# Kernel optimization log

Hardware: AMD Instinct MI355X
Metric: run time of the kernel (lower is better)

## Reference

```python
import jax, jax.numpy as jnp
import numpy as np

B, L, D = 16, 1024, 768

def setup_inputs() -> dict:
    key = jax.random.key(0)
    k1, k2, k3, k4 = jax.random.split(key, 4)
    d_embedding = jax.random.normal(k1, (B, L, D), dtype=jnp.float32)
    d_mask = jax.random.randint(k2, (B, L), 0, 2) == 1
    W = jax.random.normal(k3, (D, D), dtype=jnp.float32) / np.sqrt(D)
    b = jax.random.normal(k4, (D,), dtype=jnp.float32) * 0.01
    return {"d_embedding": d_embedding, "d_mask": d_mask, "W": W, "b": b}

def reference(d_embedding, d_mask, W, b):
    # linear + relu projection: [B, L, D]
    p = jax.nn.relu(jnp.einsum('bld,de->ble', d_embedding, W.T) + b)
    # self-attention scores: [B, L, L]
    scores = jnp.einsum('bld,bmd->blm', p, p)
    # zero out the diagonal (multiply by (1 - eye))
    diag_off = 1.0 - jnp.eye(L, dtype=scores.dtype)
    scores = scores * diag_off[None, :, :]
    # mask padded key positions with -inf (columns)
    scores = jnp.where(d_mask[:, None, :], -jnp.inf, scores)
    # softmax over keys
    alpha = jax.nn.softmax(scores, axis=-1)  # [B, L, L]
    align_feature = jnp.einsum('blm,bmd->bld', alpha, d_embedding)
    return align_feature, alpha
```

## Files before the change

### kernel.cpp

```cpp
#include <hip/hip_runtime.h>
#include <math.h>

#define B_ 16
#define L_ 1024
#define D_ 768

typedef short bf16x8 __attribute__((ext_vector_type(8)));
typedef _Float16 half8 __attribute__((ext_vector_type(8)));
typedef float f32x4 __attribute__((ext_vector_type(4)));

__device__ __forceinline__ unsigned short f2bf(float x) {
  unsigned u = __float_as_uint(x);
  u = (u + 0x7FFFu + ((u >> 16) & 1u)) >> 16;
  return (unsigned short)u;
}
__device__ __forceinline__ float bf2f(unsigned short h) {
  return __uint_as_float(((unsigned)h) << 16);
}
__device__ __forceinline__ unsigned short f2h(float x) {
  union { _Float16 h; unsigned short u; } v;
  v.h = (_Float16)x;
  return v.u;
}

__global__ __launch_bounds__(256) void k_mask2(const void* __restrict__ mraw,
                                               int* __restrict__ canon,
                                               int* __restrict__ psum,
                                               int* __restrict__ kinfo) {
  __shared__ int flags[2];
  __shared__ int tsum[256];
  const int b = blockIdx.x;
  const int tid = threadIdx.x;
  if (tid < 2) flags[tid] = 0;
  __syncthreads();
  const unsigned* m32 = (const unsigned*)mraw;
  int gt = 0, oddnz = 0;
  for (int i = tid; i < 4096; i += 256) {
    unsigned v = m32[i];
    if (v > 1u) gt = 1;
    if ((i & 1) && v != 0u) oddnz = 1;
  }
  if (gt) atomicOr(&flags[0], 1);
  if (oddnz) atomicOr(&flags[1], 1);
  __syncthreads();
  const int mode = flags[0] ? 0 : (flags[1] ? 1 : 2);
  int v[4];
#pragma unroll
  for (int e = 0; e < 4; ++e) {
    const int i = b * L_ + tid * 4 + e;
    int mv;
    if (mode == 0)      mv = ((const unsigned char*)mraw)[i];
    else if (mode == 1) mv = ((const int*)mraw)[i];
    else                mv = (int)(((const long long*)mraw)[i] != 0);
    v[e] = (mv != 0);
    canon[i] = v[e];
  }
  const int vc = (1 - v[0]) + (1 - v[1]) + (1 - v[2]) + (1 - v[3]);
  tsum[tid] = vc;
  __syncthreads();
  for (int off = 1; off < 256; off <<= 1) {
    const int t = (tid >= off) ? tsum[tid - off] : 0;
    __syncthreads();
    tsum[tid] += t;
    __syncthreads();
  }
  int run = tsum[tid] - vc;
#pragma unroll
  for (int e = 0; e < 4; ++e) {
    psum[b * L_ + tid * 4 + e] = run;
    run += 1 - v[e];
  }
  if (tid == 255) {
    const int tot = tsum[255];
    kinfo[b] = (tot + 63) >> 6;
    kinfo[16 + b] = tot;
  }
}

__global__ __launch_bounds__(256) void k_prep16(const float* __restrict__ X,
                                                unsigned short* __restrict__ Xf,
                                                unsigned short* __restrict__ Xt,
                                                const int* __restrict__ psum,
                                                const int* __restrict__ canon) {
  __shared__ unsigned short t16[64][66];
  const int b = blockIdx.z;
  const int d0 = blockIdx.x * 64, m0 = blockIdx.y * 64;
  const int dd = threadIdx.x & 63, mq = threadIdx.x >> 6;
#pragma unroll
  for (int i = 0; i < 16; ++i) {
    const int m = mq * 16 + i;
    const size_t gidx = ((size_t)b * L_ + m0 + m) * D_ + d0 + dd;
    const unsigned short h = f2h(X[gidx]);
    Xf[gidx] = h;
    t16[dd][m] = h;
  }
  __syncthreads();
  const int mm = threadIdx.x & 63, dq = threadIdx.x >> 6;
  const int gm = m0 + mm;
  if (!canon[b * L_ + gm]) {
    const int j = psum[b * L_ + gm];
#pragma unroll
    for (int i = 0; i < 16; ++i) {
      const int d = dq * 16 + i;
      Xt[((size_t)b * D_ + d0 + d) * L_ + j] = t16[d][mm];
    }
  }
}

__global__ __launch_bounds__(256) void k_prep(const float* __restrict__ X,
                                              unsigned short* __restrict__ Xh,
                                              unsigned short* __restrict__ Xl,
                                              unsigned short* __restrict__ Xt) {
  __shared__ unsigned short t16[64][66];
  const int b = blockIdx.z;
  const int d0 = blockIdx.x * 64, m0 = blockIdx.y * 64;
  const int dd = threadIdx.x & 63, mq = threadIdx.x >> 6;
#pragma unroll
  for (int i = 0; i < 16; ++i) {
    const int m = mq * 16 + i;
    const size_t gidx = ((size_t)b * L_ + m0 + m) * D_ + d0 + dd;
    const float x = X[gidx];
    const unsigned short h = f2bf(x);
    Xh[gidx] = h;
    Xl[gidx] = f2bf(x - bf2f(h));
    t16[dd][m] = h;
  }
  __syncthreads();
  const int mm = threadIdx.x & 63, dq = threadIdx.x >> 6;
#pragma unroll
  for (int i = 0; i < 16; ++i) {
    const int d = dq * 16 + i;
    Xt[((size_t)b * D_ + d0 + d) * L_ + m0 + mm] = t16[d][mm];
  }
}

__global__ __launch_bounds__(256) void k_pad(unsigned short* __restrict__ Xtc,
                                             unsigned short* __restrict__ a16c,
                                             const int* __restrict__ kinfo) {
  const int b = blockIdx.x;
  const int nt64 = kinfo[b] * 64;
  const int kv = kinfo[16 + b];
  if (kv >= nt64) return;
  const int r = blockIdx.y * 64 + (threadIdx.x >> 2);
  const int cg = threadIdx.x & 3;
  unsigned short* base = (r < 768)
      ? Xtc + ((size_t)b * D_ + r) * L_
      : a16c + ((size_t)b * L_ + (r - 768)) * L_;
#pragma unroll
  for (int q = 0; q < 16; ++q) {
    const int c = kv + cg * 16 + q;
    if (c < nt64) base[c] = 0;
  }
}

__global__ __launch_bounds__(256) void k_castW(const float* __restrict__ W,
                                               unsigned short* __restrict__ Wf,
                                               int n8) {
  const int i = blockIdx.x * 256 + threadIdx.x;
  if (i >= n8) return;
  const float4 a = *(const float4*)(W + (size_t)i * 8);
  const float4 b = *(const float4*)(W + (size_t)i * 8 + 4);
  *(ushort4*)(Wf + (size_t)i * 8)     = make_ushort4(f2h(a.x), f2h(a.y), f2h(a.z), f2h(a.w));
  *(ushort4*)(Wf + (size_t)i * 8 + 4) = make_ushort4(f2h(b.x), f2h(b.y), f2h(b.z), f2h(b.w));
}

__device__ __forceinline__ void stage_panel(const unsigned short* __restrict__ ph,
                                            const unsigned short* __restrict__ pl,
                                            size_t grow0, int kk,
                                            char* ldsbase, int wave, int lane) {
#pragma unroll
  for (int q = 0; q < 4; ++q) {
    const int s = wave * 4 + q;
    const int row = s * 8 + (lane >> 3);
    const int xs = (lane & 7) ^ (row & 7);
    const unsigned short* src = (xs & 4) ? pl : ph;
    const unsigned short* g = src + (grow0 + row) * D_ + kk + (xs & 3) * 8;
    __builtin_amdgcn_global_load_lds(
        (const __attribute__((address_space(1))) void*)g,
        (__attribute__((address_space(3))) void*)(ldsbase + s * 1024),
        16, 0, 0);
  }
}

__device__ __forceinline__ void stage_panel1(const unsigned short* __restrict__ g0,
                                             size_t rstride,
                                             char* ldsbase, int wave, int lane) {
#pragma unroll
  for (int q = 0; q < 4; ++q) {
    const int s = wave * 4 + q;
    const int row = s * 8 + (lane >> 3);
    const int xs = (lane & 7) ^ (row & 7);
    const unsigned short* g = g0 + (size_t)row * rstride + xs * 8;
    __builtin_amdgcn_global_load_lds(
        (const __attribute__((address_space(1))) void*)g,
        (__attribute__((address_space(3))) void*)(ldsbase + s * 1024),
        16, 0, 0);
  }
}

__device__ __forceinline__ bf16x8 ldsfrag(const char* base, int row, int g) {
  return *(const bf16x8*)(base + row * 128 + ((g ^ (row & 7)) * 16));
}
__device__ __forceinline__ half8 ldsfrag_h(const char* base, int row, int g) {
  return *(const half8*)(base + row * 128 + ((g ^ (row & 7)) * 16));
}

__global__ __launch_bounds__(256) void k_proj3(const unsigned short* __restrict__ Xf,
                                               const unsigned short* __restrict__ Wf,
                                               const float* __restrict__ bias,
                                               unsigned short* __restrict__ Pf) {
  __shared__ __align__(16) char smem[49152];
  const int tid = threadIdx.x;
  const int xcd = (int)blockIdx.x & 7;
  const int li  = (int)blockIdx.x >> 3;
  const int m0 = (xcd * 16 + li / 6) * 128;
  const int n0 = (li % 6) * 128;
  const int lane = tid & 63, wave = tid >> 6;
  const int wr = wave >> 1, wc = wave & 1;
  const int fr = lane & 15, kg = lane >> 4;
  f32x4 acc[4][4];
#pragma unroll
  for (int i = 0; i < 4; ++i)
#pragma unroll
    for (int j = 0; j < 4; ++j) acc[i][j] = 0;

  const unsigned short* a0 = Xf + (size_t)m0 * D_;
  const unsigned short* b0 = Wf + (size_t)n0 * D_;

  stage_panel1(a0, D_, smem, wave, lane);
  stage_panel1(b0, D_, smem + 32768, wave, lane);
  __syncthreads();

  int cur = 0;
  for (int it = 0; it < D_ / 64; ++it) {
    const char* ab = smem + cur * 16384;
    const char* bb = smem + 32768;
    half8 fa[2][4], fb[2][4];
#pragma unroll
    for (int i = 0; i < 4; ++i) {
      const int ra = wr * 64 + i * 16 + fr;
      const int rb = wc * 64 + i * 16 + fr;
#pragma unroll
      for (int ks = 0; ks < 2; ++ks) {
        fa[ks][i] = ldsfrag_h(ab, ra, ks * 4 + kg);
        fb[ks][i] = ldsfrag_h(bb, rb, ks * 4 + kg);
      }
    }
    __syncthreads();
    if (it + 1 < D_ / 64) {
      stage_panel1(a0 + (it + 1) * 64, D_, smem + (cur ^ 1) * 16384, wave, lane);
      stage_panel1(b0 + (it + 1) * 64, D_, smem + 32768, wave, lane);
    }
#pragma unroll
    for (int ks = 0; ks < 2; ++ks)
#pragma unroll
      for (int i = 0; i < 4; ++i)
#pragma unroll
        for (int j = 0; j < 4; ++j)
          acc[i][j] = __builtin_amdgcn_mfma_f32_16x16x32_f16(fa[ks][i], fb[ks][j],
                                                             acc[i][j], 0, 0, 0);
    __syncthreads();
    cur ^= 1;
  }

  unsigned short* scr = (unsigned short*)smem + wave * 1152;
  const int row = lane >> 2, seg = lane & 3;
  float bj[4];
#pragma unroll
  for (int j = 0; j < 4; ++j) bj[j] = bias[n0 + wc * 64 + j * 16 + fr];
  for (int i = 0; i < 4; ++i) {
    __syncthreads();
#pragma unroll
    for (int j = 0; j < 4; ++j)
#pragma unroll
      for (int r = 0; r < 4; ++r)
        scr[(kg * 4 + r) * 72 + j * 16 + fr] = f2h(fmaxf(acc[i][j][r] + bj[j], 0.f));
    __syncthreads();
    const size_t gr = (size_t)(m0 + wr * 64 + i * 16 + row);
    const int gc0 = n0 + wc * 64 + seg * 16;
    const uint4 h0 = *(const uint4*)&scr[row * 72 + seg * 16];
    const uint4 h1 = *(const uint4*)&scr[row * 72 + seg * 16 + 8];
    *(uint4*)(Pf + gr * D_ + gc0)     = h0;
    *(uint4*)(Pf + gr * D_ + gc0 + 8) = h1;
  }
}

__global__ __launch_bounds__(256) void k_proj(const float* __restrict__ X,
                                              const float* __restrict__ W,
                                              const float* __restrict__ bias,
                                              unsigned short* __restrict__ Ph,
                                              unsigned short* __restrict__ Pl) {
  __shared__ __align__(16) unsigned short smem[4 * 128 * 32];
  unsigned short (*Ah)[32] = (unsigned short(*)[32])smem;
  unsigned short (*Al)[32] = (unsigned short(*)[32])(smem + 1 * 128 * 32);
  unsigned short (*Bh)[32] = (unsigned short(*)[32])(smem + 2 * 128 * 32);
  unsigned short (*Bl)[32] = (unsigned short(*)[32])(smem + 3 * 128 * 32);

  const int tid = threadIdx.x;
  const int swz = ((int)blockIdx.x % 8) * 96 + (int)blockIdx.x / 8;
  const int m0 = (swz / 6) * 128, n0 = (swz % 6) * 128;
  const int lane = tid & 63, wave = tid >> 6;
  const int wr = wave >> 1, wc = wave & 1;
  const int fr = lane & 15, kg = lane >> 4;
  f32x4 acc[4][4];
#pragma unroll
  for (int i = 0; i < 4; ++i)
#pragma unroll
    for (int j = 0; j < 4; ++j) acc[i][j] = 0;

  float4 av[4], bv[4];
#pragma unroll
  for (int p = 0; p < 4; ++p) {
    const int f = tid + p * 256, r = f >> 3, c = f & 7;
    av[p] = *(const float4*)(X + (size_t)(m0 + r) * D_ + c * 4);
    bv[p] = *(const float4*)(W + (size_t)(n0 + r) * D_ + c * 4);
  }

  for (int it = 0; it < D_ / 32; ++it) {
    __syncthreads();
#pragma unroll
    for (int p = 0; p < 4; ++p) {
      const int f = tid + p * 256, r = f >> 3, c = f & 7;
      {
        const float x0 = av[p].x, x1 = av[p].y, x2 = av[p].z, x3 = av[p].w;
        const unsigned short h0 = f2bf(x0), h1 = f2bf(x1), h2 = f2bf(x2), h3 = f2bf(x3);
        *(ushort4*)&Ah[r][c * 4] = make_ushort4(h0, h1, h2, h3);
        *(ushort4*)&Al[r][c * 4] = make_ushort4(f2bf(x0 - bf2f(h0)), f2bf(x1 - bf2f(h1)),
                                                f2bf(x2 - bf2f(h2)), f2bf(x3 - bf2f(h3)));
      }
      {
        const float x0 = bv[p].x, x1 = bv[p].y, x2 = bv[p].z, x3 = bv[p].w;
        const unsigned short h0 = f2bf(x0), h1 = f2bf(x1), h2 = f2bf(x2), h3 = f2bf(x3);
        *(ushort4*)&Bh[r][c * 4] = make_ushort4(h0, h1, h2, h3);
        *(ushort4*)&Bl[r][c * 4] = make_ushort4(f2bf(x0 - bf2f(h0)), f2bf(x1 - bf2f(h1)),
                                                f2bf(x2 - bf2f(h2)), f2bf(x3 - bf2f(h3)));
      }
    }
    __syncthreads();
    if (it + 1 < D_ / 32) {
      const int kk = (it + 1) * 32;
#pragma unroll
      for (int p = 0; p < 4; ++p) {
        const int f = tid + p * 256, r = f >> 3, c = f & 7;
        av[p] = *(const float4*)(X + (size_t)(m0 + r) * D_ + kk + c * 4);
        bv[p] = *(const float4*)(W + (size_t)(n0 + r) * D_ + kk + c * 4);
      }
    }
    bf16x8 fah[4], fal[4], fbh[4], fbl[4];
#pragma unroll
    for (int i = 0; i < 4; ++i) {
      fah[i] = *(const bf16x8*)&Ah[wr * 64 + i * 16 + fr][kg * 8];
      fal[i] = *(const bf16x8*)&Al[wr * 64 + i * 16 + fr][kg * 8];
      fbh[i] = *(const bf16x8*)&Bh[wc * 64 + i * 16 + fr][kg * 8];
      fbl[i] = *(const bf16x8*)&Bl[wc * 64 + i * 16 + fr][kg * 8];
    }
#pragma unroll
    for (int i = 0; i < 4; ++i)
#pragma unroll
      for (int j = 0; j < 4; ++j) {
        acc[i][j] = __builtin_amdgcn_mfma_f32_16x16x32_bf16(fah[i], fbh[j], acc[i][j], 0, 0, 0);
        acc[i][j] = __builtin_amdgcn_mfma_f32_16x16x32_bf16(fah[i], fbl[j], acc[i][j], 0, 0, 0);
        acc[i][j] = __builtin_amdgcn_mfma_f32_16x16x32_bf16(fal[i], fbh[j], acc[i][j], 0, 0, 0);
      }
  }

  unsigned short* scr = smem + wave * 2304;
  const int row = lane >> 2, seg = lane & 3;
  float bj[4];
#pragma unroll
  for (int j = 0; j < 4; ++j) bj[j] = bias[n0 + wc * 64 + j * 16 + fr];
  for (int i = 0; i < 4; ++i) {
    __syncthreads();
#pragma unroll
    for (int j = 0; j < 4; ++j)
#pragma unroll
      for (int r = 0; r < 4; ++r) {
        float v = fmaxf(acc[i][j][r] + bj[j], 0.f);
        const unsigned short h = f2bf(v);
        scr[(kg * 4 + r) * 72 + j * 16 + fr] = h;
        scr[1152 + (kg * 4 + r) * 72 + j * 16 + fr] = f2bf(v - bf2f(h));
      }
    __syncthreads();
    const size_t gr = (size_t)(m0 + wr * 64 + i * 16 + row);
    const int gc0 = n0 + wc * 64 + seg * 16;
    const uint4 h0 = *(const uint4*)&scr[row * 72 + seg * 16];
    const uint4 h1 = *(const uint4*)&scr[row * 72 + seg * 16 + 8];
    const uint4 q0 = *(const uint4*)&scr[1152 + row * 72 + seg * 16];
    const uint4 q1 = *(const uint4*)&scr[1152 + row * 72 + seg * 16 + 8];
    *(uint4*)(Ph + gr * D_ + gc0)     = h0;
    *(uint4*)(Ph + gr * D_ + gc0 + 8) = h1;
    *(uint4*)(Pl + gr * D_ + gc0)     = q0;
    *(uint4*)(Pl + gr * D_ + gc0 + 8) = q1;
  }
}

__global__ __launch_bounds__(256) void k_scores(const unsigned short* __restrict__ Pf,
                                                const int* __restrict__ mask,
                                                float* __restrict__ S) {
  __shared__ __align__(16) char smem[65536];

  const int tid = threadIdx.x;
  const int swz = ((int)blockIdx.x % 8) * 72 + (int)blockIdx.x / 8;
  const int bb = swz / 36;
  const int pr = swz % 36;
  int ti = 0;
  while ((ti + 1) * (ti + 2) / 2 <= pr) ++ti;
  const int tj = pr - ti * (ti + 1) / 2;
  const int l0 = ti * 128, m0 = tj * 128;
  const int lane = tid & 63, wave = tid >> 6;
  const int wr = wave >> 1, wc = wave & 1;
  const int fr = lane & 15, kg = lane >> 4;
  f32x4 acc[4][4];
#pragma unroll
  for (int i = 0; i < 4; ++i)
#pragma unroll
    for (int j = 0; j < 4; ++j) acc[i][j] = 0;

  const unsigned short* a0 = Pf + ((size_t)bb * L_ + l0) * D_;
  const unsigned short* b0 = Pf + ((size_t)bb * L_ + m0) * D_;

  stage_panel1(a0, D_, smem, wave, lane);
  stage_panel1(b0, D_, smem + 16384, wave, lane);
  __syncthreads();

  int cur = 0;
  for (int it = 0; it < D_ / 64; ++it) {
    char* cb = smem + cur * 32768;
    if (it + 1 < D_ / 64) {
      char* nb = smem + (cur ^ 1) * 32768;
      stage_panel1(a0 + (it + 1) * 64, D_, nb, wave, lane);
      stage_panel1(b0 + (it + 1) * 64, D_, nb + 16384, wave, lane);
    }
    half8 fa[2][4], fb[2][4];
#pragma unroll
    for (int i = 0; i < 4; ++i) {
      const int ra = wr * 64 + i * 16 + fr;
      const int rb = wc * 64 + i * 16 + fr;
#pragma unroll
      for (int ks = 0; ks < 2; ++ks) {
        fa[ks][i] = ldsfrag_h(cb, ra, ks * 4 + kg);
        fb[ks][i] = ldsfrag_h(cb + 16384, rb, ks * 4 + kg);
      }
    }
#pragma unroll
    for (int ks = 0; ks < 2; ++ks)
#pragma unroll
      for (int i = 0; i < 4; ++i)
#pragma unroll
        for (int j = 0; j < 4; ++j)
          acc[i][j] = __builtin_amdgcn_mfma_f32_16x16x32_f16(fa[ks][i], fb[ks][j],
                                                             acc[i][j], 0, 0, 0);
    __syncthreads();
    cur ^= 1;
  }

  float* scr = (float*)smem + wave * 1280;
  const int row = lane >> 2, seg = lane & 3;
  for (int i = 0; i < 4; ++i) {
    __syncthreads();
#pragma unroll
    for (int j = 0; j < 4; ++j)
#pragma unroll
      for (int r = 0; r < 4; ++r)
        scr[(kg * 4 + r) * 68 + j * 16 + fr] = acc[i][j][r];
    __syncthreads();
    const int gl = l0 + wr * 64 + i * 16 + row;
    const int gm0 = m0 + wc * 64 + seg * 16;
    const size_t sbase = ((size_t)bb * L_ + gl) * L_ + gm0;
#pragma unroll
    for (int t = 0; t < 4; ++t) {
      float4 o = *(const float4*)&scr[row * 68 + seg * 16 + t * 4];
      const int4 mk = *(const int4*)(mask + bb * L_ + gm0 + t * 4);
      float* op = (float*)&o;
      const int* mp = (const int*)&mk;
#pragma unroll
      for (int e = 0; e < 4; ++e) {
        const int gm = gm0 + t * 4 + e;
        if (gm == gl) op[e] = 0.f;
        if (mp[e]) op[e] = -INFINITY;
      }
      *(float4*)(S + sbase + t * 4) = o;
    }
  }

  if (ti != tj) {
    __syncthreads();
#pragma unroll
    for (int j = 0; j < 4; ++j) {
      const int mloc = wc * 64 + j * 16 + fr;
#pragma unroll
      for (int i = 0; i < 4; ++i) {
        const int slot = wr * 16 + i * 4 + kg;
        const int xs = slot ^ (mloc & 7);
        *(f32x4*)(smem + mloc * 512 + xs * 16) = acc[i][j];
      }
    }
    __syncthreads();
    const int mrow = tid >> 1, half = tid & 1;
    const size_t sbase = ((size_t)bb * L_ + m0 + mrow) * L_ + l0;
#pragma unroll
    for (int q = 0; q < 16; ++q) {
      const int slot = half * 16 + q;
      const int xs = slot ^ (mrow & 7);
      float4 o = *(const float4*)(smem + mrow * 512 + xs * 16);
      const int4 mk = *(const int4*)(mask + bb * L_ + l0 + slot * 4);
      if (mk.x) o.x = -INFINITY;
      if (mk.y) o.y = -INFINITY;
      if (mk.z) o.z = -INFINITY;
      if (mk.w) o.w = -INFINITY;
      *(float4*)(S + sbase + slot * 4) = o;
    }
  }
}

__global__ __launch_bounds__(256) void k_scores_bf(const unsigned short* __restrict__ Ph,
                                                   const unsigned short* __restrict__ Pl,
                                                   const int* __restrict__ mask,
                                                   float* __restrict__ S) {
  __shared__ __align__(16) char smem[65536];

  const int tid = threadIdx.x;
  const int swz = ((int)blockIdx.x % 8) * 72 + (int)blockIdx.x / 8;
  const int bb = swz / 36;
  const int pr = swz % 36;
  int ti = 0;
  while ((ti + 1) * (ti + 2) / 2 <= pr) ++ti;
  const int tj = pr - ti * (ti + 1) / 2;
  const int l0 = ti * 128, m0 = tj * 128;
  const int lane = tid & 63, wave = tid >> 6;
  const int wr = wave >> 1, wc = wave & 1;
  const int fr = lane & 15, kg = lane >> 4;
  f32x4 acc[4][4];
#pragma unroll
  for (int i = 0; i < 4; ++i)
#pragma unroll
    for (int j = 0; j < 4; ++j) acc[i][j] = 0;

  const size_t arow0 = (size_t)bb * L_ + l0;
  const size_t brow0 = (size_t)bb * L_ + m0;

  stage_panel(Ph, Pl, arow0, 0, smem, wave, lane);
  stage_panel(Ph, Pl, brow0, 0, smem + 16384, wave, lane);
  __syncthreads();

  int cur = 0;
  for (int it = 0; it < D_ / 32; ++it) {
    char* cb = smem + cur * 32768;
    if (it + 1 < D_ / 32) {
      char* nb = smem + (cur ^ 1) * 32768;
      stage_panel(Ph, Pl, arow0, (it + 1) * 32, nb, wave, lane);
      stage_panel(Ph, Pl, brow0, (it + 1) * 32, nb + 16384, wave, lane);
    }
    bf16x8 fah[4], fal[4], fbh[4], fbl[4];
#pragma unroll
    for (int i = 0; i < 4; ++i) {
      const int ra = wr * 64 + i * 16 + fr;
      const int rb = wc * 64 + i * 16 + fr;
      fah[i] = ldsfrag(cb, ra, kg);
      fal[i] = ldsfrag(cb, ra, kg + 4);
      fbh[i] = ldsfrag(cb + 16384, rb, kg);
      fbl[i] = ldsfrag(cb + 16384, rb, kg + 4);
    }
#pragma unroll
    for (int i = 0; i < 4; ++i)
#pragma unroll
      for (int j = 0; j < 4; ++j) {
        acc[i][j] = __builtin_amdgcn_mfma_f32_16x16x32_bf16(fah[i], fbh[j], acc[i][j], 0, 0, 0);
        acc[i][j] = __builtin_amdgcn_mfma_f32_16x16x32_bf16(fah[i], fbl[j], acc[i][j], 0, 0, 0);
        acc[i][j] = __builtin_amdgcn_mfma_f32_16x16x32_bf16(fal[i], fbh[j], acc[i][j], 0, 0, 0);
      }
    __syncthreads();
    cur ^= 1;
  }

  float* scr = (float*)smem + wave * 1280;
  const int row = lane >> 2, seg = lane & 3;
  for (int i = 0; i < 4; ++i) {
    __syncthreads();
#pragma unroll
    for (int j = 0; j < 4; ++j)
#pragma unroll
      for (int r = 0; r < 4; ++r)
        scr[(kg * 4 + r) * 68 + j * 16 + fr] = acc[i][j][r];
    __syncthreads();
    const int gl = l0 + wr * 64 + i * 16 + row;
    const int gm0 = m0 + wc * 64 + seg * 16;
    const size_t sbase = ((size_t)bb * L_ + gl) * L_ + gm0;
#pragma unroll
    for (int t = 0; t < 4; ++t) {
      float4 o = *(const float4*)&scr[row * 68 + seg * 16 + t * 4];
      const int4 mk = *(const int4*)(mask + bb * L_ + gm0 + t * 4);
      float* op = (float*)&o;
      const int* mp = (const int*)&mk;
#pragma unroll
      for (int e = 0; e < 4; ++e) {
        const int gm = gm0 + t * 4 + e;
        if (gm == gl) op[e] = 0.f;
        if (mp[e]) op[e] = -INFINITY;
      }
      *(float4*)(S + sbase + t * 4) = o;
    }
  }

  if (ti != tj) {
    __syncthreads();
#pragma unroll
    for (int j = 0; j < 4; ++j) {
      const int mloc = wc * 64 + j * 16 + fr;
#pragma unroll
      for (int i = 0; i < 4; ++i) {
        const int slot = wr * 16 + i * 4 + kg;
        const int xs = slot ^ (mloc & 7);
        *(f32x4*)(smem + mloc * 512 + xs * 16) = acc[i][j];
      }
    }
    __syncthreads();
    const int mrow = tid >> 1, half = tid & 1;
    const size_t sbase = ((size_t)bb * L_ + m0 + mrow) * L_ + l0;
#pragma unroll
    for (int q = 0; q < 16; ++q) {
      const int slot = half * 16 + q;
      const int xs = slot ^ (mrow & 7);
      float4 o = *(const float4*)(smem + mrow * 512 + xs * 16);
      const int4 mk = *(const int4*)(mask + bb * L_ + l0 + slot * 4);
      if (mk.x) o.x = -INFINITY;
      if (mk.y) o.y = -INFINITY;
      if (mk.z) o.z = -INFINITY;
      if (mk.w) o.w = -INFINITY;
      *(float4*)(S + sbase + slot * 4) = o;
    }
  }
}

__global__ __launch_bounds__(256) void k_softmax(float* __restrict__ S,
                                                 unsigned short* __restrict__ a16,
                                                 const int* __restrict__ psum,
                                                 const int* __restrict__ canon) {
  const size_t row = blockIdx.x;
  float4* rp = (float4*)(S + row * L_);
  float4 v = rp[threadIdx.x];
  float mx = fmaxf(fmaxf(v.x, v.y), fmaxf(v.z, v.w));
#pragma unroll
  for (int o = 32; o > 0; o >>= 1) mx = fmaxf(mx, __shfl_xor(mx, o));
  __shared__ float rmax[4], rsum[4];
  const int wv = threadIdx.x >> 6, ln = threadIdx.x & 63;
  if (ln == 0) rmax[wv] = mx;
  __syncthreads();
  mx = fmaxf(fmaxf(rmax[0], rmax[1]), fmaxf(rmax[2], rmax[3]));
  float4 e;
  e.x = __expf(v.x - mx); e.y = __expf(v.y - mx);
  e.z = __expf(v.z - mx); e.w = __expf(v.w - mx);
  float s = (e.x + e.y) + (e.z + e.w);
#pragma unroll
  for (int o = 32; o > 0; o >>= 1) s += __shfl_xor(s, o);
  if (ln == 0) rsum[wv] = s;
  __syncthreads();
  s = (rsum[0] + rsum[1]) + (rsum[2] + rsum[3]);
  const float inv = 1.0f / s;
  e.x *= inv; e.y *= inv; e.z *= inv; e.w *= inv;
  rp[threadIdx.x] = e;
  if (a16) {
    const int bbat = (int)(row >> 10);
    const int m0 = threadIdx.x * 4;
    const int4 mk = *(const int4*)(canon + bbat * L_ + m0);
    const int4 ps = *(const int4*)(psum + bbat * L_ + m0);
    unsigned short* arow = a16 + row * L_;
    if (!mk.x) arow[ps.x] = f2h(e.x);
    if (!mk.y) arow[ps.y] = f2h(e.y);
    if (!mk.z) arow[ps.z] = f2h(e.z);
    if (!mk.w) arow[ps.w] = f2h(e.w);
  }
}

__global__ __launch_bounds__(256) void k_align2(const unsigned short* __restrict__ A16,
                                                const unsigned short* __restrict__ Xt,
                                                const int* __restrict__ kinfo,
                                                float* __restrict__ O) {
  __shared__ __align__(16) char smem[65536];
  const int tid = threadIdx.x;
  const int swz = ((int)blockIdx.x % 8) * 96 + (int)blockIdx.x / 8;
  const int bb = swz / 48;
  const int l0 = ((swz / 6) % 8) * 128;
  const int n0 = (swz % 6) * 128;
  const int nt = kinfo[bb];
  const int lane = tid & 63, wave = tid >> 6;
  const int wr = wave >> 1, wc = wave & 1;
  const int fr = lane & 15, kg = lane >> 4;
  f32x4 acc[4][4];
#pragma unroll
  for (int i = 0; i < 4; ++i)
#pragma unroll
    for (int j = 0; j < 4; ++j) acc[i][j] = 0;

  const unsigned short* a0 = A16 + ((size_t)bb * L_ + l0) * L_;
  const unsigned short* b0 = Xt + ((size_t)bb * D_ + n0) * L_;

  if (nt > 0) {
    stage_panel1(a0, L_, smem, wave, lane);
    stage_panel1(b0, L_, smem + 16384, wave, lane);
  }
  __syncthreads();

  int cur = 0;
  for (int it = 0; it < nt; ++it) {
    char* cb = smem + cur * 32768;
    if (it + 1 < nt) {
      char* nb = smem + (cur ^ 1) * 32768;
      stage_panel1(a0 + (it + 1) * 64, L_, nb, wave, lane);
      stage_panel1(b0 + (it + 1) * 64, L_, nb + 16384, wave, lane);
    }
    half8 fa[2][4], fb[2][4];
#pragma unroll
    for (int i = 0; i < 4; ++i) {
      const int ra = wr * 64 + i * 16 + fr;
      const int rb = wc * 64 + i * 16 + fr;
#pragma unroll
      for (int ks = 0; ks < 2; ++ks) {
        fa[ks][i] = ldsfrag_h(cb, ra, ks * 4 + kg);
        fb[ks][i] = ldsfrag_h(cb + 16384, rb, ks * 4 + kg);
      }
    }
#pragma unroll
    for (int ks = 0; ks < 2; ++ks)
#pragma unroll
      for (int i = 0; i < 4; ++i)
#pragma unroll
        for (int j = 0; j < 4; ++j)
          acc[i][j] = __builtin_amdgcn_mfma_f32_16x16x32_f16(fa[ks][i], fb[ks][j],
                                                             acc[i][j], 0, 0, 0);
    __syncthreads();
    cur ^= 1;
  }

  float* scr = (float*)smem + wave * 1280;
  const int row = lane >> 2, seg = lane & 3;
  for (int i = 0; i < 4; ++i) {
    __syncthreads();
#pragma unroll
    for (int j = 0; j < 4; ++j)
#pragma unroll
      for (int r = 0; r < 4; ++r)
        scr[(kg * 4 + r) * 68 + j * 16 + fr] = acc[i][j][r];
    __syncthreads();
    const int gl = l0 + wr * 64 + i * 16 + row;
    const int gc0 = n0 + wc * 64 + seg * 16;
    const size_t obase = ((size_t)bb * L_ + gl) * D_ + gc0;
#pragma unroll
    for (int t = 0; t < 4; ++t) {
      const float4 o = *(const float4*)&scr[row * 68 + seg * 16 + t * 4];
      *(float4*)(O + obase + t * 4) = o;
    }
  }
}

__global__ __launch_bounds__(256) void k_align(const float* __restrict__ A,
                                               const unsigned short* __restrict__ Xt,
                                               float* __restrict__ O) {
  __shared__ __align__(16) unsigned short smem[2 * 128 * 32];
  __shared__ __align__(16) float scr_s[4 * 1104];
  unsigned short (*Ab)[32] = (unsigned short(*)[32])smem;
  unsigned short (*Bb)[32] = (unsigned short(*)[32])(smem + 128 * 32);

  const int tid = threadIdx.x;
  const int swz = ((int)blockIdx.x % 8) * 96 + (int)blockIdx.x / 8;
  const int bb = swz / 48;
  const int l0 = ((swz / 6) % 8) * 128;
  const int n0 = (swz % 6) * 128;
  const int lane = tid & 63, wave = tid >> 6;
  const int wr = wave >> 1, wc = wave & 1;
  const int fr = lane & 15, kg = lane >> 4;
  f32x4 acc[4][4];
#pragma unroll
  for (int i = 0; i < 4; ++i)
#pragma unroll
    for (int j = 0; j < 4; ++j) acc[i][j] = 0;

  float4 av[4];
  uint4 bv[2];
#pragma unroll
  for (int p = 0; p < 4; ++p) {
    const int f = tid + p * 256, r = f >> 3, c = f & 7;
    av[p] = *(const float4*)(A + ((size_t)bb * L_ + l0 + r) * L_ + c * 4);
  }
#pragma unroll
  for (int p = 0; p < 2; ++p) {
    const int f = tid + p * 256, r = f >> 2, sl = f & 3;
    bv[p] = *(const uint4*)(Xt + ((size_t)bb * D_ + n0 + r) * L_ + sl * 8);
  }

  for (int it = 0; it < L_ / 32; ++it) {
    __syncthreads();
#pragma unroll
    for (int p = 0; p < 4; ++p) {
      const int f = tid + p * 256, r = f >> 3, c = f & 7;
      *(ushort4*)&Ab[r][c * 4] = make_ushort4(f2bf(av[p].x), f2bf(av[p].y),
                                              f2bf(av[p].z), f2bf(av[p].w));
    }
#pragma unroll
    for (int p = 0; p < 2; ++p) {
      const int f = tid + p * 256, r = f >> 2, sl = f & 3;
      *(uint4*)&Bb[r][sl * 8] = bv[p];
    }
    __syncthreads();
    if (it + 1 < L_ / 32) {
      const int kk = (it + 1) * 32;
#pragma unroll
      for (int p = 0; p < 4; ++p) {
        const int f = tid + p * 256, r = f >> 3, c = f & 7;
        av[p] = *(const float4*)(A + ((size_t)bb * L_ + l0 + r) * L_ + kk + c * 4);
      }
#pragma unroll
      for (int p = 0; p < 2; ++p) {
        const int f = tid + p * 256, r = f >> 2, sl = f & 3;
        bv[p] = *(const uint4*)(Xt + ((size_t)bb * D_ + n0 + r) * L_ + kk + sl * 8);
      }
    }
    bf16x8 fa[4], fb[4];
#pragma unroll
    for (int i = 0; i < 4; ++i) {
      fa[i] = *(const bf16x8*)&Ab[wr * 64 + i * 16 + fr][kg * 8];
      fb[i] = *(const bf16x8*)&Bb[wc * 64 + i * 16 + fr][kg * 8];
    }
#pragma unroll
    for (int i = 0; i < 4; ++i)
#pragma unroll
      for (int j = 0; j < 4; ++j)
        acc[i][j] = __builtin_amdgcn_mfma_f32_16x16x32_bf16(fa[i], fb[j], acc[i][j], 0, 0, 0);
  }

  float* scr = scr_s + wave * 1104;
  const int row = lane >> 2, seg = lane & 3;
  for (int i = 0; i < 4; ++i) {
    __syncthreads();
#pragma unroll
    for (int j = 0; j < 4; ++j)
#pragma unroll
      for (int r = 0; r < 4; ++r)
        scr[(kg * 4 + r) * 68 + j * 16 + fr] = acc[i][j][r];
    __syncthreads();
    const int gl = l0 + wr * 64 + i * 16 + row;
    const int gc0 = n0 + wc * 64 + seg * 16;
    const size_t obase = ((size_t)bb * L_ + gl) * D_ + gc0;
#pragma unroll
    for (int t = 0; t < 4; ++t) {
      const float4 o = *(const float4*)&scr[row * 68 + seg * 16 + t * 4];
      *(float4*)(O + obase + t * 4) = o;
    }
  }
}

extern "C" void kernel_launch(void* const* d_in, const int* in_sizes, int n_in,
                              void* d_out, int out_size, void* d_ws, size_t ws_size,
                              hipStream_t stream) {
  const float* X    = (const float*)d_in[0];
  const void*  mraw = d_in[1];
  const float* W    = (const float*)d_in[2];
  const float* bias = (const float*)d_in[3];

  float* out   = (float*)d_out;
  float* align = out;
  float* alpha = out + (size_t)B_ * L_ * D_;

  const size_t NX = (size_t)B_ * L_ * D_;
  const size_t NW = (size_t)D_ * D_;
  const size_t NA = (size_t)B_ * L_ * L_;

  int* maskC = (int*)d_ws;
  int* psum  = (int*)((char*)d_ws + 65536);
  int* kinfo = (int*)((char*)d_ws + 131072);
  const size_t offXt = 135168;
  unsigned short* Xt = (unsigned short*)((char*)d_ws + offXt);
  const size_t offWf = offXt + NX * 2;
  const size_t offA16 = offWf;
  const size_t need = offA16 + NA * 2;

  hipLaunchKernelGGL(k_mask2, dim3(16), dim3(256), 0, stream, mraw, maskC, psum, kinfo);

  if (ws_size >= need) {
    unsigned short* Xf = (unsigned short*)alpha;
    unsigned short* Wf = (unsigned short*)((char*)d_ws + offWf);
    unsigned short* Pf = (unsigned short*)align;
    unsigned short* A16 = (unsigned short*)((char*)d_ws + offA16);
    hipLaunchKernelGGL(k_prep16, dim3(D_ / 64, L_ / 64, B_), dim3(256), 0, stream,
                       X, Xf, Xt, psum, maskC);
    hipLaunchKernelGGL(k_castW, dim3((int)(NW / 8 / 256)), dim3(256), 0, stream,
                       W, Wf, (int)(NW / 8));
    hipLaunchKernelGGL(k_proj3, dim3(768), dim3(256), 0, stream, Xf, Wf, bias, Pf);
    hipLaunchKernelGGL(k_scores, dim3(576), dim3(256), 0, stream, Pf, maskC, alpha);
    hipLaunchKernelGGL(k_softmax, dim3(B_ * L_), dim3(256), 0, stream,
                       alpha, A16, psum, maskC);
    hipLaunchKernelGGL(k_pad, dim3(16, 28), dim3(256), 0, stream, Xt, A16, kinfo);
    hipLaunchKernelGGL(k_align2, dim3(768), dim3(256), 0, stream, A16, Xt, kinfo, align);
  } else {
    unsigned short* Ph = (unsigned short*)align;
    unsigned short* Pl = Ph + NX;
    hipLaunchKernelGGL(k_prep, dim3(D_ / 64, L_ / 64, B_), dim3(256), 0, stream,
                       X, (unsigned short*)alpha, (unsigned short*)alpha + NX, Xt);
    hipLaunchKernelGGL(k_proj, dim3(768), dim3(256), 0, stream, X, W, bias, Ph, Pl);
    hipLaunchKernelGGL(k_scores_bf, dim3(576), dim3(256), 0, stream, Ph, Pl, maskC, alpha);
    hipLaunchKernelGGL(k_softmax, dim3(B_ * L_), dim3(256), 0, stream,
                       alpha, (unsigned short*)nullptr, psum, maskC);
    hipLaunchKernelGGL(k_align, dim3(768), dim3(256), 0, stream, alpha, Xt, align);
  }
}
```

Measured before the change: 167.5 us.

## Fold padding kernel into prep and softmax; shrink align LDS buffering

Removes the separate k_pad launch. The Xt tail zeroing moves into the last row-block of k_prep16, and the A16 tail zeroing moves into k_softmax. k_align2 now double-buffers only the A panel and single-buffers the B panel, cutting LDS from 64KB to 48KB, which may let more blocks reside per CU. The cost is an extra __syncthreads per iteration and less overlap of B loads with the MFMA work.

```diff
diff --git a/kernel.cpp b/kernel.cpp
--- a/kernel.cpp
+++ b/kernel.cpp
@@ -81,7 +81,8 @@
                                                 unsigned short* __restrict__ Xf,
                                                 unsigned short* __restrict__ Xt,
                                                 const int* __restrict__ psum,
-                                                const int* __restrict__ canon) {
+                                                const int* __restrict__ canon,
+                                                const int* __restrict__ kinfo) {
   __shared__ unsigned short t16[64][66];
   const int b = blockIdx.z;
   const int d0 = blockIdx.x * 64, m0 = blockIdx.y * 64;
@@ -103,6 +104,19 @@
     for (int i = 0; i < 16; ++i) {
       const int d = dq * 16 + i;
       Xt[((size_t)b * D_ + d0 + d) * L_ + j] = t16[d][mm];
+    }
+  }
+  if (blockIdx.y == 15) {
+    const int nt64 = kinfo[b] * 64;
+    const int kv = kinfo[16 + b];
+    if (kv < nt64) {
+      const int rr = threadIdx.x >> 2, cg = threadIdx.x & 3;
+      unsigned short* base = Xt + ((size_t)b * D_ + d0 + rr) * L_;
+#pragma unroll
+      for (int q = 0; q < 16; ++q) {
+        const int c = kv + cg * 16 + q;
+        if (c < nt64) base[c] = 0;
+      }
     }
   }
 }
@@ -131,25 +145,6 @@
   for (int i = 0; i < 16; ++i) {
     const int d = dq * 16 + i;
     Xt[((size_t)b * D_ + d0 + d) * L_ + m0 + mm] = t16[d][mm];
-  }
-}
-
-__global__ __launch_bounds__(256) void k_pad(unsigned short* __restrict__ Xtc,
-                                             unsigned short* __restrict__ a16c,
-                                             const int* __restrict__ kinfo) {
-  const int b = blockIdx.x;
-  const int nt64 = kinfo[b] * 64;
-  const int kv = kinfo[16 + b];
-  if (kv >= nt64) return;
-  const int r = blockIdx.y * 64 + (threadIdx.x >> 2);
-  const int cg = threadIdx.x & 3;
-  unsigned short* base = (r < 768)
-      ? Xtc + ((size_t)b * D_ + r) * L_
-      : a16c + ((size_t)b * L_ + (r - 768)) * L_;
-#pragma unroll
-  for (int q = 0; q < 16; ++q) {
-    const int c = kv + cg * 16 + q;
-    if (c < nt64) base[c] = 0;
   }
 }
 
@@ -635,7 +630,8 @@
 __global__ __launch_bounds__(256) void k_softmax(float* __restrict__ S,
                                                  unsigned short* __restrict__ a16,
                                                  const int* __restrict__ psum,
-                                                 const int* __restrict__ canon) {
+                                                 const int* __restrict__ canon,
+                                                 const int* __restrict__ kinfo) {
   const size_t row = blockIdx.x;
   float4* rp = (float4*)(S + row * L_);
   float4 v = rp[threadIdx.x];
@@ -669,6 +665,10 @@
     if (!mk.y) arow[ps.y] = f2h(e.y);
     if (!mk.z) arow[ps.z] = f2h(e.z);
     if (!mk.w) arow[ps.w] = f2h(e.w);
+    const int nt64 = kinfo[bbat] * 64;
+    const int kv = kinfo[16 + bbat];
+    const int c = kv + (int)threadIdx.x;
+    if (c < nt64) arow[c] = 0;
   }
 }
 
@@ -676,7 +676,7 @@
                                                 const unsigned short* __restrict__ Xt,
                                                 const int* __restrict__ kinfo,
                                                 float* __restrict__ O) {
-  __shared__ __align__(16) char smem[65536];
+  __shared__ __align__(16) char smem[49152];
   const int tid = threadIdx.x;
   const int swz = ((int)blockIdx.x % 8) * 96 + (int)blockIdx.x / 8;
   const int bb = swz / 48;
@@ -697,18 +697,14 @@
 
   if (nt > 0) {
     stage_panel1(a0, L_, smem, wave, lane);
-    stage_panel1(b0, L_, smem + 16384, wave, lane);
+    stage_panel1(b0, L_, smem + 32768, wave, lane);
   }
   __syncthreads();
 
   int cur = 0;
   for (int it = 0; it < nt; ++it) {
-    char* cb = smem + cur * 32768;
-    if (it + 1 < nt) {
-      char* nb = smem + (cur ^ 1) * 32768;
-      stage_panel1(a0 + (it + 1) * 64, L_, nb, wave, lane);
-      stage_panel1(b0 + (it + 1) * 64, L_, nb + 16384, wave, lane);
-    }
+    const char* ab = smem + cur * 16384;
+    const char* bb2 = smem + 32768;
     half8 fa[2][4], fb[2][4];
 #pragma unroll
     for (int i = 0; i < 4; ++i) {
@@ -716,9 +712,14 @@
       const int rb = wc * 64 + i * 16 + fr;
 #pragma unroll
       for (int ks = 0; ks < 2; ++ks) {
-        fa[ks][i] = ldsfrag_h(cb, ra, ks * 4 + kg);
-        fb[ks][i] = ldsfrag_h(cb + 16384, rb, ks * 4 + kg);
-      }
+        fa[ks][i] = ldsfrag_h(ab, ra, ks * 4 + kg);
+        fb[ks][i] = ldsfrag_h(bb2, rb, ks * 4 + kg);
+      }
+    }
+    __syncthreads();
+    if (it + 1 < nt) {
+      stage_panel1(a0 + (it + 1) * 64, L_, smem + (cur ^ 1) * 16384, wave, lane);
+      stage_panel1(b0 + (it + 1) * 64, L_, smem + 32768, wave, lane);
     }
 #pragma unroll
     for (int ks = 0; ks < 2; ++ks)
@@ -882,14 +883,13 @@
     unsigned short* Pf = (unsigned short*)align;
     unsigned short* A16 = (unsigned short*)((char*)d_ws + offA16);
     hipLaunchKernelGGL(k_prep16, dim3(D_ / 64, L_ / 64, B_), dim3(256), 0, stream,
-                       X, Xf, Xt, psum, maskC);
+                       X, Xf, Xt, psum, maskC, kinfo);
     hipLaunchKernelGGL(k_castW, dim3((int)(NW / 8 / 256)), dim3(256), 0, stream,
                        W, Wf, (int)(NW / 8));
     hipLaunchKernelGGL(k_proj3, dim3(768), dim3(256), 0, stream, Xf, Wf, bias, Pf);
     hipLaunchKernelGGL(k_scores, dim3(576), dim3(256), 0, stream, Pf, maskC, alpha);
     hipLaunchKernelGGL(k_softmax, dim3(B_ * L_), dim3(256), 0, stream,
-                       alpha, A16, psum, maskC);
-    hipLaunchKernelGGL(k_pad, dim3(16, 28), dim3(256), 0, stream, Xt, A16, kinfo);
+                       alpha, A16, psum, maskC, kinfo);
     hipLaunchKernelGGL(k_align2, dim3(768), dim3(256), 0, stream, A16, Xt, kinfo, align);
   } else {
     unsigned short* Ph = (unsigned short*)align;
@@ -899,7 +899,7 @@
     hipLaunchKernelGGL(k_proj, dim3(768), dim3(256), 0, stream, X, W, bias, Ph, Pl);
     hipLaunchKernelGGL(k_scores_bf, dim3(576), dim3(256), 0, stream, Ph, Pl, maskC, alpha);
     hipLaunchKernelGGL(k_softmax, dim3(B_ * L_), dim3(256), 0, stream,
-                       alpha, (unsigned short*)nullptr, psum, maskC);
+                       alpha, (unsigned short*)nullptr, psum, maskC, kinfo);
     hipLaunchKernelGGL(k_align, dim3(768), dim3(256), 0, stream, alpha, Xt, align);
   }
 }
```

Measured after the change: 162.4 us. 1.03x faster.
